# Kernel tuning notes

Hardware: AMD Instinct MI355X
Metric: run time of the kernel (lower is better)

The kernel has to match this reference:

```python
import jax, jax.numpy as jnp
import numpy as np

B, Q, K, H, D = 2, 2048, 2048, 16, 64


def setup_inputs() -> dict:
    key = jax.random.key(0)
    k1, k2, k3, k4 = jax.random.split(key, 4)
    qs = jax.random.normal(k1, (B, Q, H, D), dtype=jnp.float32)
    ks = jax.random.normal(k2, (B, K, H, D), dtype=jnp.float32)
    vs = jax.random.normal(k3, (B, K, H, D), dtype=jnp.float32)
    # valid lengths in [1, K] so no row is fully masked
    valid_lens = jax.random.randint(k4, (B,), 1, K + 1, dtype=jnp.int32)
    return {"qs": qs, "ks": ks, "vs": vs, "valid_lens": valid_lens}


def reference(qs, ks, vs, valid_lens):
    # Flash-attention-2 scan computes exact softmax attention with key masking;
    # the dense, numerically-stable equivalent:
    d = qs.shape[-1]
    scale = 1.0 / jnp.sqrt(jnp.asarray(d, dtype=qs.dtype))
    # scores: [B, H, Q, K]
    scores = jnp.einsum("bqhd,bkhd->bhqk", qs * scale, ks)
    kpos = jnp.arange(ks.shape[1])
    ks_mask = kpos[None, :] < valid_lens[:, None]            # [B, K]
    scores = jnp.where(ks_mask[:, None, None, :], scores, -jnp.inf)
    attn = jax.nn.softmax(scores, axis=-1)                   # stable online-softmax equivalent
    out = jnp.einsum("bhqk,bkhd->bqhd", attn, vs)            # [B, Q, H, D]
    return out
```

## Files before the change

kernel.cpp:

```cpp
#include <hip/hip_runtime.h>

#define B_ 2
#define Q_ 2048
#define K_ 2048
#define H_ 16
#define D_ 64
#define HD_ (H_ * D_)

#define QSCALE 0.18033688011112042f
#define DEFER_THR 10.0f

typedef __bf16 bf16_t;
typedef __attribute__((ext_vector_type(8))) __bf16 bf16x8;
typedef __attribute__((ext_vector_type(4))) __bf16 bf16x4;
typedef __attribute__((ext_vector_type(4))) float f32x4;

#define SBAR() do {                                         \
    __builtin_amdgcn_sched_barrier(0);                      \
    asm volatile("s_waitcnt lgkmcnt(0)" ::: "memory");      \
    __builtin_amdgcn_s_barrier();                           \
    __builtin_amdgcn_sched_barrier(0);                      \
} while (0)

__device__ __forceinline__ int swz(int row, int colByte) {
    return (row * 128 + colByte) ^ ((row & 7) << 4);
}

__global__ __launch_bounds__(512, 4) void attn_fwd_kernel(
    const float* __restrict__ qs, const float* __restrict__ ks,
    const float* __restrict__ vs, const int* __restrict__ valid_lens,
    float* __restrict__ out)
{
    const int qt   = blockIdx.x;
    const int h    = blockIdx.y;
    const int b    = blockIdx.z;
    const int tid  = threadIdx.x;
    const int wave = tid >> 6;
    const int lane = tid & 63;
    const int l16  = lane & 15;
    const int lhi  = lane >> 4;

    const int valid  = valid_lens[b];
    const int ntiles = (valid + 63) >> 6;

    __shared__ bf16_t k_lds[2][64 * 64];
    __shared__ bf16_t v_lds[2][64 * 64];
    __shared__ bf16_t p_buf[8][16 * 64];
    char* const pbase = (char*)&p_buf[wave][0];

    const int    qrow = qt * 128 + wave * 16 + l16;
    const float* qp   = qs + (((size_t)b * Q_ + qrow) * H_ + h) * D_;
    bf16x8 a_q[2];
    #pragma unroll
    for (int dh = 0; dh < 2; ++dh) {
        const f32x4* q4 = (const f32x4*)(qp + dh * 32 + lhi * 8);
        f32x4 lo = q4[0], hi = q4[1];
        #pragma unroll
        for (int j = 0; j < 4; ++j) {
            a_q[dh][j]     = (bf16_t)(lo[j] * QSCALE);
            a_q[dh][4 + j] = (bf16_t)(hi[j] * QSCALE);
        }
    }

    f32x4 o_acc[4];
    #pragma unroll
    for (int t = 0; t < 4; ++t) o_acc[t] = (f32x4){0.f, 0.f, 0.f, 0.f};
    float m_r[4], l_part[4];
    #pragma unroll
    for (int r = 0; r < 4; ++r) { m_r[r] = -1e30f; l_part[r] = 0.f; }

    const float* kb = ks + ((size_t)b * K_ * H_ + h) * D_;
    const float* vg = vs + ((size_t)b * K_ * H_ + h) * D_;

    const bool kRole = (tid < 256);
    const int  st    = kRole ? tid : (tid - 256);
    const int  krow  = st >> 2;
    const int  kcolf = (st & 3) * 16;
    const int  vr    = (st & 15) * 4;
    const int  vc    = (st >> 4) * 4;

    f32x4 reg[4];

    auto issue_loads = [&](int kt) {
        if (kRole) {
            const float* ksrc = kb + (size_t)(kt * 64 + krow) * HD_ + kcolf;
            #pragma unroll
            for (int i = 0; i < 4; ++i) reg[i] = ((const f32x4*)ksrc)[i];
        } else {
            #pragma unroll
            for (int i = 0; i < 4; ++i)
                reg[i] = *(const f32x4*)(vg + (size_t)(kt * 64 + vr + i) * HD_ + vc);
        }
    };

    auto write_tile = [&](int bi) {
        if (kRole) {
            char* kdst = (char*)&k_lds[bi][0];
            bf16x8 lo, hi;
            #pragma unroll
            for (int j = 0; j < 4; ++j) {
                lo[j] = (bf16_t)reg[0][j]; lo[4 + j] = (bf16_t)reg[1][j];
                hi[j] = (bf16_t)reg[2][j]; hi[4 + j] = (bf16_t)reg[3][j];
            }
            *(bf16x8*)(kdst + swz(krow, kcolf * 2))      = lo;
            *(bf16x8*)(kdst + swz(krow, kcolf * 2 + 16)) = hi;
        } else {
            char* vdst = (char*)&v_lds[bi][0];
            #pragma unroll
            for (int j = 0; j < 4; ++j) {
                bf16x4 w;
                w[0] = (bf16_t)reg[0][j]; w[1] = (bf16_t)reg[1][j];
                w[2] = (bf16_t)reg[2][j]; w[3] = (bf16_t)reg[3][j];
                *(bf16x4*)(vdst + swz(vc + j, vr * 2)) = w;
            }
        }
    };

    issue_loads(0);
    write_tile(0);
    int cur = 0;

    for (int kt = 0; kt < ntiles; ++kt) {
        const bool more = (kt + 1 < ntiles);
        if (more) issue_loads(kt + 1);
        SBAR();

        char* const kbase = (char*)&k_lds[cur][0];
        char* const vbase = (char*)&v_lds[cur][0];

        f32x4 s[4];
        #pragma unroll
        for (int n = 0; n < 4; ++n) s[n] = (f32x4){0.f, 0.f, 0.f, 0.f};
        __builtin_amdgcn_s_setprio(1);
        #pragma unroll
        for (int n = 0; n < 4; ++n) {
            #pragma unroll
            for (int dh = 0; dh < 2; ++dh) {
                bf16x8 bk = *(const bf16x8*)(kbase + swz(n * 16 + l16, dh * 64 + lhi * 16));
                s[n] = __builtin_amdgcn_mfma_f32_16x16x32_bf16(a_q[dh], bk, s[n], 0, 0, 0);
            }
        }
        __builtin_amdgcn_s_setprio(0);

        if (kt * 64 + 64 > valid) {
            #pragma unroll
            for (int n = 0; n < 4; ++n) {
                const bool ok = (kt * 64 + n * 16 + l16) < valid;
                #pragma unroll
                for (int r = 0; r < 4; ++r)
                    if (!ok) s[n][r] = -1e30f;
            }
        }

        float lm[4];
        bool need = false;
        #pragma unroll
        for (int r = 0; r < 4; ++r) {
            lm[r] = fmaxf(fmaxf(s[0][r], s[1][r]), fmaxf(s[2][r], s[3][r]));
            need = need || (lm[r] > m_r[r] + DEFER_THR);
        }
        if (__any(need)) {
            #pragma unroll
            for (int r = 0; r < 4; ++r) {
                float rm = lm[r];
                #pragma unroll
                for (int off = 1; off < 16; off <<= 1)
                    rm = fmaxf(rm, __shfl_xor(rm, off, 64));
                const float mnew = fmaxf(m_r[r], rm);
                const float alpha = __builtin_amdgcn_exp2f(m_r[r] - mnew);
                m_r[r] = mnew;
                l_part[r] *= alpha;
                #pragma unroll
                for (int t = 0; t < 4; ++t) o_acc[t][r] *= alpha;
            }
        }
        #pragma unroll
        for (int r = 0; r < 4; ++r) {
            float psum = 0.f;
            #pragma unroll
            for (int n = 0; n < 4; ++n) {
                const float e = __builtin_amdgcn_exp2f(s[n][r] - m_r[r]);
                psum += e;
                *(bf16_t*)(pbase + swz(lhi * 4 + r, (n * 16 + l16) * 2)) = (bf16_t)e;
            }
            l_part[r] += psum;
        }

        bf16x8 pa[2];
        #pragma unroll
        for (int kk = 0; kk < 2; ++kk)
            pa[kk] = *(const bf16x8*)(pbase + swz(l16, kk * 64 + lhi * 16));

        __builtin_amdgcn_s_setprio(1);
        #pragma unroll
        for (int t = 0; t < 4; ++t) {
            #pragma unroll
            for (int kk = 0; kk < 2; ++kk) {
                bf16x8 vb = *(const bf16x8*)(vbase + swz(t * 16 + l16, kk * 64 + lhi * 16));
                o_acc[t] = __builtin_amdgcn_mfma_f32_16x16x32_bf16(pa[kk], vb, o_acc[t], 0, 0, 0);
            }
        }
        __builtin_amdgcn_s_setprio(0);

        if (more) write_tile(cur ^ 1);
        cur ^= 1;
    }

    float* op = out + (((size_t)b * Q_ + qt * 128 + wave * 16) * H_ + h) * D_;
    #pragma unroll
    for (int r = 0; r < 4; ++r) {
        float l = l_part[r];
        #pragma unroll
        for (int off = 1; off < 16; off <<= 1)
            l += __shfl_xor(l, off, 64);
        const int   row = lhi * 4 + r;
        const float inv = 1.f / l;
        #pragma unroll
        for (int t = 0; t < 4; ++t)
            op[(size_t)row * HD_ + t * 16 + l16] = o_acc[t][r] * inv;
    }
}

extern "C" void kernel_launch(void* const* d_in, const int* in_sizes, int n_in,
                              void* d_out, int out_size, void* d_ws, size_t ws_size,
                              hipStream_t stream) {
    const float* qs = (const float*)d_in[0];
    const float* ks = (const float*)d_in[1];
    const float* vs = (const float*)d_in[2];
    const int*   vl = (const int*)d_in[3];
    float*       out = (float*)d_out;
    dim3 grid(Q_ / 128, H_, B_);
    attn_fwd_kernel<<<grid, 512, 0, stream>>>(qs, ks, vs, vl, out);
}
```

Before: 41.44 us.

## Transpose MFMA operands so each lane owns one query row's scores

After: 39.11 us. 5.6% less time.

```diff
diff --git a/kernel.cpp b/kernel.cpp
--- a/kernel.cpp
+++ b/kernel.cpp
@@ -65,9 +65,7 @@
     f32x4 o_acc[4];
     #pragma unroll
     for (int t = 0; t < 4; ++t) o_acc[t] = (f32x4){0.f, 0.f, 0.f, 0.f};
-    float m_r[4], l_part[4];
-    #pragma unroll
-    for (int r = 0; r < 4; ++r) { m_r[r] = -1e30f; l_part[r] = 0.f; }
+    float m_r = -1e30f, l_part = 0.f;
 
     const float* kb = ks + ((size_t)b * K_ * H_ + h) * D_;
     const float* vg = vs + ((size_t)b * K_ * H_ + h) * D_;
@@ -136,8 +134,8 @@
         for (int n = 0; n < 4; ++n) {
             #pragma unroll
             for (int dh = 0; dh < 2; ++dh) {
-                bf16x8 bk = *(const bf16x8*)(kbase + swz(n * 16 + l16, dh * 64 + lhi * 16));
-                s[n] = __builtin_amdgcn_mfma_f32_16x16x32_bf16(a_q[dh], bk, s[n], 0, 0, 0);
+                bf16x8 ak = *(const bf16x8*)(kbase + swz(n * 16 + l16, dh * 64 + lhi * 16));
+                s[n] = __builtin_amdgcn_mfma_f32_16x16x32_bf16(ak, a_q[dh], s[n], 0, 0, 0);
             }
         }
         __builtin_amdgcn_s_setprio(0);
@@ -145,51 +143,46 @@
         if (kt * 64 + 64 > valid) {
             #pragma unroll
             for (int n = 0; n < 4; ++n) {
-                const bool ok = (kt * 64 + n * 16 + l16) < valid;
+                const int kbase_i = kt * 64 + n * 16 + lhi * 4;
                 #pragma unroll
                 for (int r = 0; r < 4; ++r)
-                    if (!ok) s[n][r] = -1e30f;
-            }
-        }
-
-        float lm[4];
-        bool need = false;
-        #pragma unroll
-        for (int r = 0; r < 4; ++r) {
-            lm[r] = fmaxf(fmaxf(s[0][r], s[1][r]), fmaxf(s[2][r], s[3][r]));
-            need = need || (lm[r] > m_r[r] + DEFER_THR);
-        }
-        if (__any(need)) {
+                    if (kbase_i + r >= valid) s[n][r] = -1e30f;
+            }
+        }
+
+        float lm = s[0][0];
+        #pragma unroll
+        for (int n = 0; n < 4; ++n)
+            #pragma unroll
+            for (int r = 0; r < 4; ++r) lm = fmaxf(lm, s[n][r]);
+        if (__any(lm > m_r + DEFER_THR)) {
+            float rm = fmaxf(lm, __shfl_xor(lm, 16, 64));
+            rm = fmaxf(rm, __shfl_xor(rm, 32, 64));
+            const float mnew  = fmaxf(m_r, rm);
+            const float alpha = __builtin_amdgcn_exp2f(m_r - mnew);
+            m_r = mnew;
+            l_part *= alpha;
+            #pragma unroll
+            for (int t = 0; t < 4; ++t) o_acc[t] *= alpha;
+        }
+        float psum = 0.f;
+        #pragma unroll
+        for (int n = 0; n < 4; ++n) {
+            bf16x4 w;
             #pragma unroll
             for (int r = 0; r < 4; ++r) {
-                float rm = lm[r];
-                #pragma unroll
-                for (int off = 1; off < 16; off <<= 1)
-                    rm = fmaxf(rm, __shfl_xor(rm, off, 64));
-                const float mnew = fmaxf(m_r[r], rm);
-                const float alpha = __builtin_amdgcn_exp2f(m_r[r] - mnew);
-                m_r[r] = mnew;
-                l_part[r] *= alpha;
-                #pragma unroll
-                for (int t = 0; t < 4; ++t) o_acc[t][r] *= alpha;
-            }
-        }
-        #pragma unroll
-        for (int r = 0; r < 4; ++r) {
-            float psum = 0.f;
-            #pragma unroll
-            for (int n = 0; n < 4; ++n) {
-                const float e = __builtin_amdgcn_exp2f(s[n][r] - m_r[r]);
+                const float e = __builtin_amdgcn_exp2f(s[n][r] - m_r);
                 psum += e;
-                *(bf16_t*)(pbase + swz(lhi * 4 + r, (n * 16 + l16) * 2)) = (bf16_t)e;
-            }
-            l_part[r] += psum;
-        }
-
-        bf16x8 pa[2];
+                w[r] = (bf16_t)e;
+            }
+            *(bf16x4*)(pbase + swz(l16, n * 32 + lhi * 8)) = w;
+        }
+        l_part += psum;
+
+        bf16x8 pb[2];
         #pragma unroll
         for (int kk = 0; kk < 2; ++kk)
-            pa[kk] = *(const bf16x8*)(pbase + swz(l16, kk * 64 + lhi * 16));
+            pb[kk] = *(const bf16x8*)(pbase + swz(l16, kk * 64 + lhi * 16));
 
         __builtin_amdgcn_s_setprio(1);
         #pragma unroll
@@ -197,7 +190,7 @@
             #pragma unroll
             for (int kk = 0; kk < 2; ++kk) {
                 bf16x8 vb = *(const bf16x8*)(vbase + swz(t * 16 + l16, kk * 64 + lhi * 16));
-                o_acc[t] = __builtin_amdgcn_mfma_f32_16x16x32_bf16(pa[kk], vb, o_acc[t], 0, 0, 0);
+                o_acc[t] = __builtin_amdgcn_mfma_f32_16x16x32_bf16(vb, pb[kk], o_acc[t], 0, 0, 0);
             }
         }
         __builtin_amdgcn_s_setprio(0);
@@ -206,18 +199,17 @@
         cur ^= 1;
     }
 
-    float* op = out + (((size_t)b * Q_ + qt * 128 + wave * 16) * H_ + h) * D_;
+    float l = l_part;
+    l += __shfl_xor(l, 16, 64);
+    l += __shfl_xor(l, 32, 64);
+    const float inv = 1.f / l;
+    float* op = out + (((size_t)b * Q_ + qrow) * H_ + h) * D_;
     #pragma unroll
-    for (int r = 0; r < 4; ++r) {
-        float l = l_part[r];
-        #pragma unroll
-        for (int off = 1; off < 16; off <<= 1)
-            l += __shfl_xor(l, off, 64);
-        const int   row = lhi * 4 + r;
-        const float inv = 1.f / l;
-        #pragma unroll
-        for (int t = 0; t < 4; ++t)
-            op[(size_t)row * HD_ + t * 16 + l16] = o_acc[t][r] * inv;
+    for (int t = 0; t < 4; ++t) {
+        f32x4 res = o_acc[t];
+        #pragma unroll
+        for (int r = 0; r < 4; ++r) res[r] *= inv;
+        *(f32x4*)(op + t * 16 + lhi * 4) = res;
     }
 }
 
```
